# Kernel optimization log

Hardware: AMD Instinct MI355X
Metric: run time of the kernel (lower is better)

## Reference

```python
import jax, jax.numpy as jnp
import numpy as np

B = 262144
EDGES_SRC = np.array([0, 0, 0, 0])
EDGES_DST = np.array([1, 2, 3, 4])
PRED_IDS = np.array([[0, 10, 14], [1, 11, 18], [2, 12, 22], [3, 13, 26]])
O_IDS = np.array([0, 1, 2, 3, 10, 11, 12, 13, 14, 18, 22, 26])


def _xavier(k, shape):
    fan_out, fan_in = shape
    bound = float(np.sqrt(6.0 / (fan_in + fan_out)))
    return jax.random.uniform(k, shape, jnp.float32, -bound, bound)


def setup_inputs() -> dict:
    key = jax.random.key(0)
    ks = jax.random.split(key, 12)
    return {
        "initial_c": jax.random.uniform(ks[0], (B, 30), jnp.float32),
        "initial_s": jax.random.normal(ks[1], (B, 9), jnp.float32),
        "current_c": jax.random.uniform(ks[2], (B, 30), jnp.float32),
        "eps": jax.random.normal(ks[3], (B, 8), jnp.float32),
        # GnnMessagePassing params (torch Linear: y = x @ W.T + b)
        "W1": _xavier(ks[4], (128, 13)), "b1": jnp.zeros(128, jnp.float32),
        "W2": _xavier(ks[5], (39, 128)), "b2": jnp.zeros(39, jnp.float32),
        "W3": _xavier(ks[6], (128, 39)), "b3": jnp.zeros(128, jnp.float32),
        "Wm": _xavier(ks[7], (8, 128)), "bm": jnp.zeros(8, jnp.float32),
        "Wv": _xavier(ks[8], (8, 128)), "bv": jnp.zeros(8, jnp.float32),
        # Decoder params: [25 -> 32 -> 12], sigmoid output (binary=True)
        "Wd1": _xavier(ks[9], (32, 25)), "bd1": jnp.zeros(32, jnp.float32),
        "Wd2": _xavier(ks[10], (12, 32)), "bd2": jnp.zeros(12, jnp.float32),
    }


def reference(initial_c, initial_s, current_c, eps,
              W1, b1, W2, b2, W3, b3, Wm, bm, Wv, bv, Wd1, bd1, Wd2, bd2):
    bsz = current_c.shape[0]
    eye = jnp.eye(5, dtype=current_c.dtype)
    # per-edge constant one-hot pair features: [4, 10]
    edge_onehot = jnp.concatenate([eye[EDGES_SRC], eye[EDGES_DST]], axis=-1)
    edge_onehot = jnp.broadcast_to(edge_onehot[:, None, :], (4, bsz, 10))
    # gather predicate triplets per edge: [B, 4, 3] -> [4, B, 3]
    preds = jnp.transpose(current_c[:, PRED_IDS], (1, 0, 2))
    inp_mp = jnp.concatenate([edge_onehot, preds], axis=-1)  # [4, B, 13]

    # message MLP + sum over edge dim
    x = jax.nn.relu(jnp.einsum('ebi,oi->ebo', inp_mp, W1) + b1)  # [4, B, 128]
    x = jax.nn.relu(jnp.einsum('ebi,oi->ebo', x, W2) + b2)       # [4, B, 39]
    x = x.sum(axis=0)                                            # [B, 39]
    x = jax.nn.relu(x @ W3.T + b3)                               # [B, 128]
    means = x @ Wm.T + bm                                        # [B, 8]
    log_var = x @ Wv.T + bv                                      # [B, 8]

    # reparameterization
    z = eps * jnp.exp(0.5 * log_var) + means

    # decoder: [one-hot(node 0) | initial_c[o_ids] | z] -> sigmoid MLP
    node0 = jnp.broadcast_to(eye[0], (bsz, 5))
    inp_dec = jnp.concatenate([node0, initial_c[:, O_IDS], z], axis=1)  # [B, 25]
    h = jax.nn.relu(inp_dec @ Wd1.T + bd1)
    recon_x = jax.nn.sigmoid(h @ Wd2.T + bd2)  # [B, 12]
    return recon_x, means, log_var, z
```

## Files before the change

kernel.cpp:

```cpp
#include <hip/hip_runtime.h>
#include <hip/hip_bf16.h>

#define TPB 256
#define PREP_BLOCKS 64

typedef __attribute__((ext_vector_type(8))) short short8;
typedef __attribute__((ext_vector_type(4))) float f32x4;

#define G_W2F   0
#define G_MVF   12288
#define G_D1F   16384
#define G_D2F   18432
#define G_CEAB  19456
#define G_B2P   23552
#define G_B3    23744
#define G_BMV   24256
#define G_D1C   24320
#define G_BD2   24448
#define G_W3F   24512
#define G_END   40896

__device__ __forceinline__ unsigned short f2bf(float f) {
    unsigned int u = __float_as_uint(f);
    unsigned int r = u + 0x7fffu + ((u >> 16) & 1u);
    return (unsigned short)(r >> 16);
}
__device__ __forceinline__ unsigned int pk(float a, float b) {
    __hip_bfloat162 h = __float22bfloat162_rn(make_float2(a, b));
    unsigned int u; __builtin_memcpy(&u, &h, 4); return u;
}

__global__ void prep_kernel(
    const float* __restrict__ W1, const float* __restrict__ b1,
    const float* __restrict__ W2, const float* __restrict__ b2,
    const float* __restrict__ W3, const float* __restrict__ b3,
    const float* __restrict__ Wm, const float* __restrict__ bm,
    const float* __restrict__ Wv, const float* __restrict__ bv,
    const float* __restrict__ Wd1, const float* __restrict__ bd1,
    const float* __restrict__ Wd2, const float* __restrict__ bd2,
    unsigned char* __restrict__ ws)
{
    const int g0 = blockIdx.x * TPB + threadIdx.x;
    const int gs = gridDim.x * TPB;
    unsigned short* w2f = (unsigned short*)(ws + G_W2F);
    for (int i = g0; i < 6144; i += gs) {
        int j = i & 7, lane = (i >> 3) & 63, ts = i >> 9;
        int t = ts >> 2, s = ts & 3, q = lane >> 4;
        int n = 16 * t + (lane & 15);
        int phys = 16 * (2 * s + (j >> 2)) + 4 * q + (j & 3);
        w2f[i] = (n < 39) ? f2bf(W2[n * 128 + phys]) : 0;
    }
    unsigned short* w3f = (unsigned short*)(ws + G_W3F);
    for (int i = g0; i < 8192; i += gs) {
        int j = i & 7, lane = (i >> 3) & 63, ns = i >> 9;
        int nt = ns >> 1, s = ns & 1, q = lane >> 4;
        int n = 16 * nt + (lane & 15);
        int phys = 16 * (2 * s + (j >> 2)) + 4 * q + (j & 3);
        w3f[i] = (phys < 39) ? f2bf(W3[n * 39 + phys]) : 0;
    }
    unsigned short* mvf = (unsigned short*)(ws + G_MVF);
    for (int i = g0; i < 2048; i += gs) {
        int j = i & 7, lane = (i >> 3) & 63, s = i >> 9;
        int q = lane >> 4, n = lane & 15;
        int phys = 16 * (2 * s + (j >> 2)) + 4 * q + (j & 3);
        mvf[i] = f2bf(n < 8 ? Wm[n * 128 + phys] : Wv[(n - 8) * 128 + phys]);
    }
    unsigned short* d1f = (unsigned short*)(ws + G_D1F);
    for (int i = g0; i < 1024; i += gs) {
        int j = i & 7, lane = (i >> 3) & 63, tt = i >> 9;
        int q = lane >> 4, n = 16 * tt + (lane & 15);
        int phys = 16 * (j >> 2) + 4 * q + (j & 3);
        d1f[i] = (phys < 20) ? f2bf(Wd1[n * 25 + 5 + phys]) : 0;
    }
    unsigned short* d2f = (unsigned short*)(ws + G_D2F);
    for (int i = g0; i < 512; i += gs) {
        int j = i & 7, lane = i >> 3;
        int q = lane >> 4, n = lane & 15;
        int phys = 16 * (j >> 2) + 4 * q + (j & 3);
        d2f[i] = (n < 12) ? f2bf(Wd2[n * 32 + phys]) : 0;
    }
    unsigned short* ceab = (unsigned short*)(ws + G_CEAB);
    for (int i = g0; i < 2048; i += gs) {
        int c = i & 3, n = (i >> 2) & 127, e = i >> 9;
        float v = (c < 3) ? W1[n * 13 + 10 + c]
                          : (W1[n * 13 + 0] + W1[n * 13 + 6 + e] + b1[n]);
        ceab[i] = f2bf(v);
    }
    float* fb = (float*)(ws + G_B2P);
    for (int i = g0; i < 48; i += gs) fb[i] = (i < 39) ? b2[i] : 0.f;
    fb = (float*)(ws + G_B3);
    for (int i = g0; i < 128; i += gs) fb[i] = b3[i];
    fb = (float*)(ws + G_BMV);
    for (int i = g0; i < 16; i += gs) fb[i] = (i < 8) ? bm[i] : bv[i - 8];
    fb = (float*)(ws + G_D1C);
    for (int i = g0; i < 32; i += gs) fb[i] = Wd1[i * 25 + 0] + bd1[i];
    fb = (float*)(ws + G_BD2);
    for (int i = g0; i < 16; i += gs) fb[i] = (i < 12) ? bd2[i] : 0.f;
}

union S8 { short8 v; uint4 u; };

#define MFMA(a, b, c) __builtin_amdgcn_mfma_f32_16x16x32_bf16(a, b, c, 0, 0, 0)

__global__ __launch_bounds__(TPB, 2) void vae_mfma(
    const float* __restrict__ ic, const float* __restrict__ cc,
    const float* __restrict__ eps,
    const unsigned char* __restrict__ ws,
    float* __restrict__ out, int B)
{
    const int tid = threadIdx.x;
    const int lane = tid & 63, w = tid >> 6;
    const int quad = lane >> 4, n16 = lane & 15;
    const bool q0 = (quad == 0);
    const long rb = ((long)blockIdx.x * 4 + w) * 16;
    const long Rl = rb + n16;

    float pa[4] = {0,0,0,0}, pb[4] = {0,0,0,0}, pc[4] = {0,0,0,0};
    if (q0) {
        const float* crow = cc + Rl * 30;
        float2 t0 = *(const float2*)(crow);
        float2 t1 = *(const float2*)(crow + 2);
        float2 t2 = *(const float2*)(crow + 10);
        float2 t3 = *(const float2*)(crow + 12);
        pa[0] = t0.x; pa[1] = t0.y; pa[2] = t1.x; pa[3] = t1.y;
        pb[0] = t2.x; pb[1] = t2.y; pb[2] = t3.x; pb[3] = t3.y;
        pc[0] = crow[14]; pc[1] = crow[18]; pc[2] = crow[22]; pc[3] = crow[26];
    }

    S8 W2F[12];
    #pragma unroll
    for (int ts = 0; ts < 12; ts++)
        W2F[ts].u = *(const uint4*)(ws + G_W2F + (ts * 64 + lane) * 16);
    const float* b2p = (const float*)(ws + G_B2P);
    f32x4 b2q[3];
    #pragma unroll
    for (int t = 0; t < 3; t++)
        b2q[t] = *(const f32x4*)(b2p + 16 * t + 4 * quad);

    f32x4 ss0 = {0,0,0,0}, ss1 = {0,0,0,0}, ss2 = {0,0,0,0};

    #pragma unroll
    for (int e = 0; e < 4; e++) {
        S8 bp;
        bp.u.x = q0 ? pk(pa[e], pb[e]) : 0u;
        bp.u.y = q0 ? pk(pc[e], 1.0f) : 0u;
        bp.u.z = 0u; bp.u.w = 0u;
        const unsigned long long* cb =
            (const unsigned long long*)(ws + G_CEAB + e * 1024);
        S8 xf[4];
        #pragma unroll
        for (int mt = 0; mt < 8; mt++) {
            unsigned long long bw = cb[mt * 16 + n16];
            S8 af;
            af.u.x = q0 ? (unsigned int)bw : 0u;
            af.u.y = q0 ? (unsigned int)(bw >> 32) : 0u;
            af.u.z = 0u; af.u.w = 0u;
            f32x4 z4 = {0,0,0,0};
            f32x4 cr = MFMA(af.v, bp.v, z4);
            unsigned int lo = pk(fmaxf(cr[0], 0.f), fmaxf(cr[1], 0.f));
            unsigned int hi = pk(fmaxf(cr[2], 0.f), fmaxf(cr[3], 0.f));
            if ((mt & 1) == 0) { xf[mt >> 1].u.x = lo; xf[mt >> 1].u.y = hi; }
            else               { xf[mt >> 1].u.z = lo; xf[mt >> 1].u.w = hi; }
        }
        f32x4 c0 = b2q[0], c1 = b2q[1], c2 = b2q[2];
        #pragma unroll
        for (int s = 0; s < 4; s++) {
            c0 = MFMA(W2F[s].v,     xf[s].v, c0);
            c1 = MFMA(W2F[4 + s].v, xf[s].v, c1);
            c2 = MFMA(W2F[8 + s].v, xf[s].v, c2);
        }
        #pragma unroll
        for (int r = 0; r < 4; r++) {
            ss0[r] += fmaxf(c0[r], 0.f);
            ss1[r] += fmaxf(c1[r], 0.f);
            ss2[r] += fmaxf(c2[r], 0.f);
        }
    }

    S8 sf0, sf1;
    sf0.u.x = pk(ss0[0], ss0[1]); sf0.u.y = pk(ss0[2], ss0[3]);
    sf0.u.z = pk(ss1[0], ss1[1]); sf0.u.w = pk(ss1[2], ss1[3]);
    sf1.u.x = pk(ss2[0], ss2[1]); sf1.u.y = pk(ss2[2], ss2[3]);
    sf1.u.z = 0u; sf1.u.w = 0u;

    const uint4* w3g = (const uint4*)(ws + G_W3F);
    const float* b3p = (const float*)(ws + G_B3);
    S8 hf[4];
    #pragma unroll
    for (int nt = 0; nt < 8; nt++) {
        f32x4 c = *(const f32x4*)(b3p + nt * 16 + 4 * quad);
        S8 a0, a1;
        a0.u = w3g[(nt * 2 + 0) * 64 + lane];
        a1.u = w3g[(nt * 2 + 1) * 64 + lane];
        c = MFMA(a0.v, sf0.v, c);
        c = MFMA(a1.v, sf1.v, c);
        unsigned int lo = pk(fmaxf(c[0], 0.f), fmaxf(c[1], 0.f));
        unsigned int hi = pk(fmaxf(c[2], 0.f), fmaxf(c[3], 0.f));
        if ((nt & 1) == 0) { hf[nt >> 1].u.x = lo; hf[nt >> 1].u.y = hi; }
        else               { hf[nt >> 1].u.z = lo; hf[nt >> 1].u.w = hi; }
    }

    f32x4 cm = *(const f32x4*)((const float*)(ws + G_BMV) + 4 * quad);
    #pragma unroll
    for (int s = 0; s < 4; s++) {
        S8 a; a.u = *(const uint4*)(ws + G_MVF + (s * 64 + lane) * 16);
        cm = MFMA(a.v, hf[s].v, cm);
    }

    const int addrLv = ((lane + 32) & 63) << 2;
    float lvv[4];
    #pragma unroll
    for (int r = 0; r < 4; r++)
        lvv[r] = __int_as_float(
            __builtin_amdgcn_ds_bpermute(addrLv, __float_as_int(cm[r])));
    float4 ev = *(const float4*)(eps + Rl * 8 + 4 * (quad & 1));
    f32x4 zz;
    zz[0] = fmaf(ev.x, __expf(0.5f * lvv[0]), cm[0]);
    zz[1] = fmaf(ev.y, __expf(0.5f * lvv[1]), cm[1]);
    zz[2] = fmaf(ev.z, __expf(0.5f * lvv[2]), cm[2]);
    zz[3] = fmaf(ev.w, __expf(0.5f * lvv[3]), cm[3]);
    float* pml = (float*)((quad < 2) ? (out + (long)B * 12) : (out + (long)B * 20));
    *(float4*)(pml + Rl * 8 + 4 * (quad & 1)) = *(float4*)&cm;
    if (quad < 2)
        *(float4*)(out + (long)B * 28 + Rl * 8 + 4 * quad) = *(float4*)&zz;

    const int addrZ = (n16 + (q0 ? 16 : 0)) << 2;
    float zr[4];
    #pragma unroll
    for (int r = 0; r < 4; r++)
        zr[r] = __int_as_float(
            __builtin_amdgcn_ds_bpermute(addrZ, __float_as_int(zz[r])));

    const float* irow = ic + Rl * 30;
    float d0, d1, d2, d3;
    if (quad == 3)      { d0 = zr[0];    d1 = zr[1];    d2 = zr[2];    d3 = zr[3]; }
    else if (quad == 2) { d0 = irow[14]; d1 = irow[18]; d2 = irow[22]; d3 = irow[26]; }
    else {
        const float* p = irow + (quad ? 10 : 0);
        float2 u0 = *(const float2*)(p);
        float2 u1 = *(const float2*)(p + 2);
        d0 = u0.x; d1 = u0.y; d2 = u1.x; d3 = u1.y;
    }
    S8 df;
    df.u.x = pk(d0, d1);
    df.u.y = pk(d2, d3);
    df.u.z = q0 ? pk(zr[0], zr[1]) : 0u;
    df.u.w = q0 ? pk(zr[2], zr[3]) : 0u;

    const float* d1c = (const float*)(ws + G_D1C);
    S8 a;
    f32x4 ct = *(const f32x4*)(d1c + 4 * quad);
    a.u = *(const uint4*)(ws + G_D1F + (0 * 64 + lane) * 16);
    f32x4 h0 = MFMA(a.v, df.v, ct);
    ct = *(const f32x4*)(d1c + 16 + 4 * quad);
    a.u = *(const uint4*)(ws + G_D1F + (1 * 64 + lane) * 16);
    f32x4 h1 = MFMA(a.v, df.v, ct);
    S8 hf2;
    hf2.u.x = pk(fmaxf(h0[0], 0.f), fmaxf(h0[1], 0.f));
    hf2.u.y = pk(fmaxf(h0[2], 0.f), fmaxf(h0[3], 0.f));
    hf2.u.z = pk(fmaxf(h1[0], 0.f), fmaxf(h1[1], 0.f));
    hf2.u.w = pk(fmaxf(h1[2], 0.f), fmaxf(h1[3], 0.f));

    f32x4 c2 = *(const f32x4*)((const float*)(ws + G_BD2) + 4 * quad);
    S8 a2; a2.u = *(const uint4*)(ws + G_D2F + lane * 16);
    c2 = MFMA(a2.v, hf2.v, c2);
    if (quad < 3) {
        float4 o;
        o.x = 1.f / (1.f + __expf(-c2[0]));
        o.y = 1.f / (1.f + __expf(-c2[1]));
        o.z = 1.f / (1.f + __expf(-c2[2]));
        o.w = 1.f / (1.f + __expf(-c2[3]));
        *(float4*)(out + Rl * 12 + 4 * quad) = o;
    }
}

extern "C" void kernel_launch(void* const* d_in, const int* in_sizes, int n_in,
                              void* d_out, int out_size, void* d_ws, size_t ws_size,
                              hipStream_t stream) {
    const float* ic  = (const float*)d_in[0];
    const float* cc  = (const float*)d_in[2];
    const float* eps = (const float*)d_in[3];

    const int B = in_sizes[3] / 8;
    const int nblocks = B / 64;

    prep_kernel<<<PREP_BLOCKS, TPB, 0, stream>>>(
        (const float*)d_in[4],  (const float*)d_in[5],
        (const float*)d_in[6],  (const float*)d_in[7],
        (const float*)d_in[8],  (const float*)d_in[9],
        (const float*)d_in[10], (const float*)d_in[11],
        (const float*)d_in[12], (const float*)d_in[13],
        (const float*)d_in[14], (const float*)d_in[15],
        (const float*)d_in[16], (const float*)d_in[17],
        (unsigned char*)d_ws);
    vae_mfma<<<nblocks, TPB, 0, stream>>>(
        ic, cc, eps, (const unsigned char*)d_ws, (float*)d_out, B);
}
```

Before: 199.2 us.

## Process two 16-row tiles per wavefront to reuse weight fragments

Each wavefront now handles 32 batch rows as two 16-row MFMA tiles. Every weight fragment load (W2, W3, Wm/Wv, decoder) feeds two MFMAs, and the two independent chains interleave. The grid is halved to match. The W2 fragments are no longer held in registers for the whole kernel but are reloaded inside the edge loop. This adds register pressure and halves the number of waves available for latency hiding.

```diff
diff --git a/kernel.cpp b/kernel.cpp
--- a/kernel.cpp
+++ b/kernel.cpp
@@ -112,42 +112,46 @@
     const int lane = tid & 63, w = tid >> 6;
     const int quad = lane >> 4, n16 = lane & 15;
     const bool q0 = (quad == 0);
-    const long rb = ((long)blockIdx.x * 4 + w) * 16;
-    const long Rl = rb + n16;
-
-    float pa[4] = {0,0,0,0}, pb[4] = {0,0,0,0}, pc[4] = {0,0,0,0};
+    const long rb = ((long)blockIdx.x * 4 + w) * 32;
+
+    unsigned int bpx[2][4] = {{0,0,0,0},{0,0,0,0}};
+    unsigned int bpy[2][4] = {{0,0,0,0},{0,0,0,0}};
     if (q0) {
-        const float* crow = cc + Rl * 30;
-        float2 t0 = *(const float2*)(crow);
-        float2 t1 = *(const float2*)(crow + 2);
-        float2 t2 = *(const float2*)(crow + 10);
-        float2 t3 = *(const float2*)(crow + 12);
-        pa[0] = t0.x; pa[1] = t0.y; pa[2] = t1.x; pa[3] = t1.y;
-        pb[0] = t2.x; pb[1] = t2.y; pb[2] = t3.x; pb[3] = t3.y;
-        pc[0] = crow[14]; pc[1] = crow[18]; pc[2] = crow[22]; pc[3] = crow[26];
-    }
-
-    S8 W2F[12];
-    #pragma unroll
-    for (int ts = 0; ts < 12; ts++)
-        W2F[ts].u = *(const uint4*)(ws + G_W2F + (ts * 64 + lane) * 16);
+        #pragma unroll
+        for (int t = 0; t < 2; t++) {
+            const float* crow = cc + (rb + 16 * t + n16) * 30;
+            float2 u0 = *(const float2*)(crow);
+            float2 u1 = *(const float2*)(crow + 2);
+            float2 u2 = *(const float2*)(crow + 10);
+            float2 u3 = *(const float2*)(crow + 12);
+            float pc0 = crow[14], pc1 = crow[18], pc2 = crow[22], pc3 = crow[26];
+            bpx[t][0] = pk(u0.x, u2.x); bpy[t][0] = pk(pc0, 1.0f);
+            bpx[t][1] = pk(u0.y, u2.y); bpy[t][1] = pk(pc1, 1.0f);
+            bpx[t][2] = pk(u1.x, u3.x); bpy[t][2] = pk(pc2, 1.0f);
+            bpx[t][3] = pk(u1.y, u3.y); bpy[t][3] = pk(pc3, 1.0f);
+        }
+    }
+
     const float* b2p = (const float*)(ws + G_B2P);
     f32x4 b2q[3];
     #pragma unroll
     for (int t = 0; t < 3; t++)
         b2q[t] = *(const f32x4*)(b2p + 16 * t + 4 * quad);
 
-    f32x4 ss0 = {0,0,0,0}, ss1 = {0,0,0,0}, ss2 = {0,0,0,0};
+    f32x4 ss0[2], ss1[2], ss2[2];
+    #pragma unroll
+    for (int t = 0; t < 2; t++) {
+        ss0[t] = (f32x4){0,0,0,0}; ss1[t] = (f32x4){0,0,0,0}; ss2[t] = (f32x4){0,0,0,0};
+    }
 
     #pragma unroll
     for (int e = 0; e < 4; e++) {
-        S8 bp;
-        bp.u.x = q0 ? pk(pa[e], pb[e]) : 0u;
-        bp.u.y = q0 ? pk(pc[e], 1.0f) : 0u;
-        bp.u.z = 0u; bp.u.w = 0u;
+        S8 bp0, bp1;
+        bp0.u.x = bpx[0][e]; bp0.u.y = bpy[0][e]; bp0.u.z = 0u; bp0.u.w = 0u;
+        bp1.u.x = bpx[1][e]; bp1.u.y = bpy[1][e]; bp1.u.z = 0u; bp1.u.w = 0u;
         const unsigned long long* cb =
             (const unsigned long long*)(ws + G_CEAB + e * 1024);
-        S8 xf[4];
+        S8 xf0[4], xf1[4];
         #pragma unroll
         for (int mt = 0; mt < 8; mt++) {
             unsigned long long bw = cb[mt * 16 + n16];
@@ -156,121 +160,163 @@
             af.u.y = q0 ? (unsigned int)(bw >> 32) : 0u;
             af.u.z = 0u; af.u.w = 0u;
             f32x4 z4 = {0,0,0,0};
-            f32x4 cr = MFMA(af.v, bp.v, z4);
-            unsigned int lo = pk(fmaxf(cr[0], 0.f), fmaxf(cr[1], 0.f));
-            unsigned int hi = pk(fmaxf(cr[2], 0.f), fmaxf(cr[3], 0.f));
-            if ((mt & 1) == 0) { xf[mt >> 1].u.x = lo; xf[mt >> 1].u.y = hi; }
-            else               { xf[mt >> 1].u.z = lo; xf[mt >> 1].u.w = hi; }
-        }
-        f32x4 c0 = b2q[0], c1 = b2q[1], c2 = b2q[2];
+            f32x4 cr0 = MFMA(af.v, bp0.v, z4);
+            f32x4 cr1 = MFMA(af.v, bp1.v, z4);
+            unsigned int lo0 = pk(fmaxf(cr0[0], 0.f), fmaxf(cr0[1], 0.f));
+            unsigned int hi0 = pk(fmaxf(cr0[2], 0.f), fmaxf(cr0[3], 0.f));
+            unsigned int lo1 = pk(fmaxf(cr1[0], 0.f), fmaxf(cr1[1], 0.f));
+            unsigned int hi1 = pk(fmaxf(cr1[2], 0.f), fmaxf(cr1[3], 0.f));
+            if ((mt & 1) == 0) {
+                xf0[mt >> 1].u.x = lo0; xf0[mt >> 1].u.y = hi0;
+                xf1[mt >> 1].u.x = lo1; xf1[mt >> 1].u.y = hi1;
+            } else {
+                xf0[mt >> 1].u.z = lo0; xf0[mt >> 1].u.w = hi0;
+                xf1[mt >> 1].u.z = lo1; xf1[mt >> 1].u.w = hi1;
+            }
+        }
+        f32x4 c00 = b2q[0], c01 = b2q[1], c02 = b2q[2];
+        f32x4 c10 = b2q[0], c11 = b2q[1], c12 = b2q[2];
         #pragma unroll
         for (int s = 0; s < 4; s++) {
-            c0 = MFMA(W2F[s].v,     xf[s].v, c0);
-            c1 = MFMA(W2F[4 + s].v, xf[s].v, c1);
-            c2 = MFMA(W2F[8 + s].v, xf[s].v, c2);
+            S8 w0, w1, w2;
+            w0.u = *(const uint4*)(ws + G_W2F + ((s) * 64 + lane) * 16);
+            w1.u = *(const uint4*)(ws + G_W2F + ((4 + s) * 64 + lane) * 16);
+            w2.u = *(const uint4*)(ws + G_W2F + ((8 + s) * 64 + lane) * 16);
+            c00 = MFMA(w0.v, xf0[s].v, c00);
+            c10 = MFMA(w0.v, xf1[s].v, c10);
+            c01 = MFMA(w1.v, xf0[s].v, c01);
+            c11 = MFMA(w1.v, xf1[s].v, c11);
+            c02 = MFMA(w2.v, xf0[s].v, c02);
+            c12 = MFMA(w2.v, xf1[s].v, c12);
         }
         #pragma unroll
         for (int r = 0; r < 4; r++) {
-            ss0[r] += fmaxf(c0[r], 0.f);
-            ss1[r] += fmaxf(c1[r], 0.f);
-            ss2[r] += fmaxf(c2[r], 0.f);
-        }
-    }
-
-    S8 sf0, sf1;
-    sf0.u.x = pk(ss0[0], ss0[1]); sf0.u.y = pk(ss0[2], ss0[3]);
-    sf0.u.z = pk(ss1[0], ss1[1]); sf0.u.w = pk(ss1[2], ss1[3]);
-    sf1.u.x = pk(ss2[0], ss2[1]); sf1.u.y = pk(ss2[2], ss2[3]);
-    sf1.u.z = 0u; sf1.u.w = 0u;
+            ss0[0][r] += fmaxf(c00[r], 0.f);
+            ss1[0][r] += fmaxf(c01[r], 0.f);
+            ss2[0][r] += fmaxf(c02[r], 0.f);
+            ss0[1][r] += fmaxf(c10[r], 0.f);
+            ss1[1][r] += fmaxf(c11[r], 0.f);
+            ss2[1][r] += fmaxf(c12[r], 0.f);
+        }
+    }
+
+    S8 sf0[2], sf1[2];
+    #pragma unroll
+    for (int t = 0; t < 2; t++) {
+        sf0[t].u.x = pk(ss0[t][0], ss0[t][1]); sf0[t].u.y = pk(ss0[t][2], ss0[t][3]);
+        sf0[t].u.z = pk(ss1[t][0], ss1[t][1]); sf0[t].u.w = pk(ss1[t][2], ss1[t][3]);
+        sf1[t].u.x = pk(ss2[t][0], ss2[t][1]); sf1[t].u.y = pk(ss2[t][2], ss2[t][3]);
+        sf1[t].u.z = 0u; sf1[t].u.w = 0u;
+    }
 
     const uint4* w3g = (const uint4*)(ws + G_W3F);
     const float* b3p = (const float*)(ws + G_B3);
-    S8 hf[4];
+    S8 hf[2][4];
     #pragma unroll
     for (int nt = 0; nt < 8; nt++) {
-        f32x4 c = *(const f32x4*)(b3p + nt * 16 + 4 * quad);
+        f32x4 cb3 = *(const f32x4*)(b3p + nt * 16 + 4 * quad);
         S8 a0, a1;
         a0.u = w3g[(nt * 2 + 0) * 64 + lane];
         a1.u = w3g[(nt * 2 + 1) * 64 + lane];
-        c = MFMA(a0.v, sf0.v, c);
-        c = MFMA(a1.v, sf1.v, c);
-        unsigned int lo = pk(fmaxf(c[0], 0.f), fmaxf(c[1], 0.f));
-        unsigned int hi = pk(fmaxf(c[2], 0.f), fmaxf(c[3], 0.f));
-        if ((nt & 1) == 0) { hf[nt >> 1].u.x = lo; hf[nt >> 1].u.y = hi; }
-        else               { hf[nt >> 1].u.z = lo; hf[nt >> 1].u.w = hi; }
-    }
-
-    f32x4 cm = *(const f32x4*)((const float*)(ws + G_BMV) + 4 * quad);
+        f32x4 c0 = cb3, c1 = cb3;
+        c0 = MFMA(a0.v, sf0[0].v, c0);
+        c1 = MFMA(a0.v, sf0[1].v, c1);
+        c0 = MFMA(a1.v, sf1[0].v, c0);
+        c1 = MFMA(a1.v, sf1[1].v, c1);
+        unsigned int lo0 = pk(fmaxf(c0[0], 0.f), fmaxf(c0[1], 0.f));
+        unsigned int hi0 = pk(fmaxf(c0[2], 0.f), fmaxf(c0[3], 0.f));
+        unsigned int lo1 = pk(fmaxf(c1[0], 0.f), fmaxf(c1[1], 0.f));
+        unsigned int hi1 = pk(fmaxf(c1[2], 0.f), fmaxf(c1[3], 0.f));
+        if ((nt & 1) == 0) {
+            hf[0][nt >> 1].u.x = lo0; hf[0][nt >> 1].u.y = hi0;
+            hf[1][nt >> 1].u.x = lo1; hf[1][nt >> 1].u.y = hi1;
+        } else {
+            hf[0][nt >> 1].u.z = lo0; hf[0][nt >> 1].u.w = hi0;
+            hf[1][nt >> 1].u.z = lo1; hf[1][nt >> 1].u.w = hi1;
+        }
+    }
+
+    f32x4 cmb = *(const f32x4*)((const float*)(ws + G_BMV) + 4 * quad);
+    f32x4 cm[2]; cm[0] = cmb; cm[1] = cmb;
     #pragma unroll
     for (int s = 0; s < 4; s++) {
         S8 a; a.u = *(const uint4*)(ws + G_MVF + (s * 64 + lane) * 16);
-        cm = MFMA(a.v, hf[s].v, cm);
-    }
+        cm[0] = MFMA(a.v, hf[0][s].v, cm[0]);
+        cm[1] = MFMA(a.v, hf[1][s].v, cm[1]);
+    }
+
+    const float* d1c = (const float*)(ws + G_D1C);
+    f32x4 ct0 = *(const f32x4*)(d1c + 4 * quad);
+    f32x4 ct1 = *(const f32x4*)(d1c + 16 + 4 * quad);
+    S8 ad10, ad11, ad2;
+    ad10.u = *(const uint4*)(ws + G_D1F + (0 * 64 + lane) * 16);
+    ad11.u = *(const uint4*)(ws + G_D1F + (1 * 64 + lane) * 16);
+    ad2.u  = *(const uint4*)(ws + G_D2F + lane * 16);
+    f32x4 bd2q = *(const f32x4*)((const float*)(ws + G_BD2) + 4 * quad);
 
     const int addrLv = ((lane + 32) & 63) << 2;
-    float lvv[4];
-    #pragma unroll
-    for (int r = 0; r < 4; r++)
-        lvv[r] = __int_as_float(
-            __builtin_amdgcn_ds_bpermute(addrLv, __float_as_int(cm[r])));
-    float4 ev = *(const float4*)(eps + Rl * 8 + 4 * (quad & 1));
-    f32x4 zz;
-    zz[0] = fmaf(ev.x, __expf(0.5f * lvv[0]), cm[0]);
-    zz[1] = fmaf(ev.y, __expf(0.5f * lvv[1]), cm[1]);
-    zz[2] = fmaf(ev.z, __expf(0.5f * lvv[2]), cm[2]);
-    zz[3] = fmaf(ev.w, __expf(0.5f * lvv[3]), cm[3]);
-    float* pml = (float*)((quad < 2) ? (out + (long)B * 12) : (out + (long)B * 20));
-    *(float4*)(pml + Rl * 8 + 4 * (quad & 1)) = *(float4*)&cm;
-    if (quad < 2)
-        *(float4*)(out + (long)B * 28 + Rl * 8 + 4 * quad) = *(float4*)&zz;
-
     const int addrZ = (n16 + (q0 ? 16 : 0)) << 2;
-    float zr[4];
-    #pragma unroll
-    for (int r = 0; r < 4; r++)
-        zr[r] = __int_as_float(
-            __builtin_amdgcn_ds_bpermute(addrZ, __float_as_int(zz[r])));
-
-    const float* irow = ic + Rl * 30;
-    float d0, d1, d2, d3;
-    if (quad == 3)      { d0 = zr[0];    d1 = zr[1];    d2 = zr[2];    d3 = zr[3]; }
-    else if (quad == 2) { d0 = irow[14]; d1 = irow[18]; d2 = irow[22]; d3 = irow[26]; }
-    else {
-        const float* p = irow + (quad ? 10 : 0);
-        float2 u0 = *(const float2*)(p);
-        float2 u1 = *(const float2*)(p + 2);
-        d0 = u0.x; d1 = u0.y; d2 = u1.x; d3 = u1.y;
-    }
-    S8 df;
-    df.u.x = pk(d0, d1);
-    df.u.y = pk(d2, d3);
-    df.u.z = q0 ? pk(zr[0], zr[1]) : 0u;
-    df.u.w = q0 ? pk(zr[2], zr[3]) : 0u;
-
-    const float* d1c = (const float*)(ws + G_D1C);
-    S8 a;
-    f32x4 ct = *(const f32x4*)(d1c + 4 * quad);
-    a.u = *(const uint4*)(ws + G_D1F + (0 * 64 + lane) * 16);
-    f32x4 h0 = MFMA(a.v, df.v, ct);
-    ct = *(const f32x4*)(d1c + 16 + 4 * quad);
-    a.u = *(const uint4*)(ws + G_D1F + (1 * 64 + lane) * 16);
-    f32x4 h1 = MFMA(a.v, df.v, ct);
-    S8 hf2;
-    hf2.u.x = pk(fmaxf(h0[0], 0.f), fmaxf(h0[1], 0.f));
-    hf2.u.y = pk(fmaxf(h0[2], 0.f), fmaxf(h0[3], 0.f));
-    hf2.u.z = pk(fmaxf(h1[0], 0.f), fmaxf(h1[1], 0.f));
-    hf2.u.w = pk(fmaxf(h1[2], 0.f), fmaxf(h1[3], 0.f));
-
-    f32x4 c2 = *(const f32x4*)((const float*)(ws + G_BD2) + 4 * quad);
-    S8 a2; a2.u = *(const uint4*)(ws + G_D2F + lane * 16);
-    c2 = MFMA(a2.v, hf2.v, c2);
-    if (quad < 3) {
-        float4 o;
-        o.x = 1.f / (1.f + __expf(-c2[0]));
-        o.y = 1.f / (1.f + __expf(-c2[1]));
-        o.z = 1.f / (1.f + __expf(-c2[2]));
-        o.w = 1.f / (1.f + __expf(-c2[3]));
-        *(float4*)(out + Rl * 12 + 4 * quad) = o;
+
+    #pragma unroll
+    for (int t = 0; t < 2; t++) {
+        const long Rt = rb + 16 * t + n16;
+
+        float lvv[4];
+        #pragma unroll
+        for (int r = 0; r < 4; r++)
+            lvv[r] = __int_as_float(
+                __builtin_amdgcn_ds_bpermute(addrLv, __float_as_int(cm[t][r])));
+        float4 ev = *(const float4*)(eps + Rt * 8 + 4 * (quad & 1));
+        f32x4 zz;
+        zz[0] = fmaf(ev.x, __expf(0.5f * lvv[0]), cm[t][0]);
+        zz[1] = fmaf(ev.y, __expf(0.5f * lvv[1]), cm[t][1]);
+        zz[2] = fmaf(ev.z, __expf(0.5f * lvv[2]), cm[t][2]);
+        zz[3] = fmaf(ev.w, __expf(0.5f * lvv[3]), cm[t][3]);
+        float* pml = (float*)((quad < 2) ? (out + (long)B * 12) : (out + (long)B * 20));
+        *(float4*)(pml + Rt * 8 + 4 * (quad & 1)) = *(float4*)&cm[t];
+        if (quad < 2)
+            *(float4*)(out + (long)B * 28 + Rt * 8 + 4 * quad) = *(float4*)&zz;
+
+        float zr[4];
+        #pragma unroll
+        for (int r = 0; r < 4; r++)
+            zr[r] = __int_as_float(
+                __builtin_amdgcn_ds_bpermute(addrZ, __float_as_int(zz[r])));
+
+        const float* irow = ic + Rt * 30;
+        float d0, d1, d2, d3;
+        if (quad == 3)      { d0 = zr[0];    d1 = zr[1];    d2 = zr[2];    d3 = zr[3]; }
+        else if (quad == 2) { d0 = irow[14]; d1 = irow[18]; d2 = irow[22]; d3 = irow[26]; }
+        else {
+            const float* p = irow + (quad ? 10 : 0);
+            float2 u0 = *(const float2*)(p);
+            float2 u1 = *(const float2*)(p + 2);
+            d0 = u0.x; d1 = u0.y; d2 = u1.x; d3 = u1.y;
+        }
+        S8 df;
+        df.u.x = pk(d0, d1);
+        df.u.y = pk(d2, d3);
+        df.u.z = q0 ? pk(zr[0], zr[1]) : 0u;
+        df.u.w = q0 ? pk(zr[2], zr[3]) : 0u;
+
+        f32x4 h0 = MFMA(ad10.v, df.v, ct0);
+        f32x4 h1 = MFMA(ad11.v, df.v, ct1);
+        S8 hf2;
+        hf2.u.x = pk(fmaxf(h0[0], 0.f), fmaxf(h0[1], 0.f));
+        hf2.u.y = pk(fmaxf(h0[2], 0.f), fmaxf(h0[3], 0.f));
+        hf2.u.z = pk(fmaxf(h1[0], 0.f), fmaxf(h1[1], 0.f));
+        hf2.u.w = pk(fmaxf(h1[2], 0.f), fmaxf(h1[3], 0.f));
+
+        f32x4 c2 = bd2q;
+        c2 = MFMA(ad2.v, hf2.v, c2);
+        if (quad < 3) {
+            float4 o;
+            o.x = 1.f / (1.f + __expf(-c2[0]));
+            o.y = 1.f / (1.f + __expf(-c2[1]));
+            o.z = 1.f / (1.f + __expf(-c2[2]));
+            o.w = 1.f / (1.f + __expf(-c2[3]));
+            *(float4*)(out + Rt * 12 + 4 * quad) = o;
+        }
     }
 }
 
@@ -282,7 +328,7 @@
     const float* eps = (const float*)d_in[3];
 
     const int B = in_sizes[3] / 8;
-    const int nblocks = B / 64;
+    const int nblocks = B / 128;
 
     prep_kernel<<<PREP_BLOCKS, TPB, 0, stream>>>(
         (const float*)d_in[4],  (const float*)d_in[5],
```

Result: faster. 192.5 us (-3.3%).

## Raise occupancy to 4 blocks per CU by reloading W2 fragments per edge

Applied to the files above, without the earlier changes.

Raises the launch bound from 2 to 4 blocks per multiprocessor. To fit the tighter register budget, the 12 W2 MFMA fragments and the b2 bias vectors are no longer held in registers for the whole kernel but reloaded from global/L2 inside each edge iteration. The predicate values are packed to bf16 pairs right after loading, so fewer live float registers are needed. The aim is better latency hiding from more waves, at the cost of four times as many weight loads, and possible spills if the compiler cannot fit the new limit.

```diff
diff --git a/kernel.cpp b/kernel.cpp
--- a/kernel.cpp
+++ b/kernel.cpp
@@ -102,7 +102,7 @@
 
 #define MFMA(a, b, c) __builtin_amdgcn_mfma_f32_16x16x32_bf16(a, b, c, 0, 0, 0)
 
-__global__ __launch_bounds__(TPB, 2) void vae_mfma(
+__global__ __launch_bounds__(TPB, 4) void vae_mfma(
     const float* __restrict__ ic, const float* __restrict__ cc,
     const float* __restrict__ eps,
     const unsigned char* __restrict__ ws,
@@ -115,36 +115,26 @@
     const long rb = ((long)blockIdx.x * 4 + w) * 16;
     const long Rl = rb + n16;
 
-    float pa[4] = {0,0,0,0}, pb[4] = {0,0,0,0}, pc[4] = {0,0,0,0};
+    unsigned int bpx[4] = {0,0,0,0}, bpy[4] = {0,0,0,0};
     if (q0) {
         const float* crow = cc + Rl * 30;
-        float2 t0 = *(const float2*)(crow);
-        float2 t1 = *(const float2*)(crow + 2);
-        float2 t2 = *(const float2*)(crow + 10);
-        float2 t3 = *(const float2*)(crow + 12);
-        pa[0] = t0.x; pa[1] = t0.y; pa[2] = t1.x; pa[3] = t1.y;
-        pb[0] = t2.x; pb[1] = t2.y; pb[2] = t3.x; pb[3] = t3.y;
-        pc[0] = crow[14]; pc[1] = crow[18]; pc[2] = crow[22]; pc[3] = crow[26];
-    }
-
-    S8 W2F[12];
-    #pragma unroll
-    for (int ts = 0; ts < 12; ts++)
-        W2F[ts].u = *(const uint4*)(ws + G_W2F + (ts * 64 + lane) * 16);
+        float2 u0 = *(const float2*)(crow);
+        float2 u1 = *(const float2*)(crow + 2);
+        float2 u2 = *(const float2*)(crow + 10);
+        float2 u3 = *(const float2*)(crow + 12);
+        bpx[0] = pk(u0.x, u2.x); bpy[0] = pk(crow[14], 1.0f);
+        bpx[1] = pk(u0.y, u2.y); bpy[1] = pk(crow[18], 1.0f);
+        bpx[2] = pk(u1.x, u3.x); bpy[2] = pk(crow[22], 1.0f);
+        bpx[3] = pk(u1.y, u3.y); bpy[3] = pk(crow[26], 1.0f);
+    }
+
     const float* b2p = (const float*)(ws + G_B2P);
-    f32x4 b2q[3];
-    #pragma unroll
-    for (int t = 0; t < 3; t++)
-        b2q[t] = *(const f32x4*)(b2p + 16 * t + 4 * quad);
-
     f32x4 ss0 = {0,0,0,0}, ss1 = {0,0,0,0}, ss2 = {0,0,0,0};
 
     #pragma unroll
     for (int e = 0; e < 4; e++) {
         S8 bp;
-        bp.u.x = q0 ? pk(pa[e], pb[e]) : 0u;
-        bp.u.y = q0 ? pk(pc[e], 1.0f) : 0u;
-        bp.u.z = 0u; bp.u.w = 0u;
+        bp.u.x = bpx[e]; bp.u.y = bpy[e]; bp.u.z = 0u; bp.u.w = 0u;
         const unsigned long long* cb =
             (const unsigned long long*)(ws + G_CEAB + e * 1024);
         S8 xf[4];
@@ -162,12 +152,18 @@
             if ((mt & 1) == 0) { xf[mt >> 1].u.x = lo; xf[mt >> 1].u.y = hi; }
             else               { xf[mt >> 1].u.z = lo; xf[mt >> 1].u.w = hi; }
         }
-        f32x4 c0 = b2q[0], c1 = b2q[1], c2 = b2q[2];
+        f32x4 c0 = *(const f32x4*)(b2p + 4 * quad);
+        f32x4 c1 = *(const f32x4*)(b2p + 16 + 4 * quad);
+        f32x4 c2 = *(const f32x4*)(b2p + 32 + 4 * quad);
         #pragma unroll
         for (int s = 0; s < 4; s++) {
-            c0 = MFMA(W2F[s].v,     xf[s].v, c0);
-            c1 = MFMA(W2F[4 + s].v, xf[s].v, c1);
-            c2 = MFMA(W2F[8 + s].v, xf[s].v, c2);
+            S8 w0, w1, w2;
+            w0.u = *(const uint4*)(ws + G_W2F + ((s) * 64 + lane) * 16);
+            w1.u = *(const uint4*)(ws + G_W2F + ((4 + s) * 64 + lane) * 16);
+            w2.u = *(const uint4*)(ws + G_W2F + ((8 + s) * 64 + lane) * 16);
+            c0 = MFMA(w0.v, xf[s].v, c0);
+            c1 = MFMA(w1.v, xf[s].v, c1);
+            c2 = MFMA(w2.v, xf[s].v, c2);
         }
         #pragma unroll
         for (int r = 0; r < 4; r++) {
```

New measurement: 253.0 us. 1.27x slower.
